# Kernel tuning notes

Hardware: AMD Instinct MI355X
Metric: run time of the kernel (lower is better)

Reference implementation:

```python
import jax, jax.numpy as jnp
import numpy as np
import math

D_K = 128
M_BYTES = 65536  # default M = 1024*64
B_C = math.ceil(M_BYTES / (4 * D_K))  # = 128 key-block size
SCALE = 1.0 / math.sqrt(D_K)


def setup_inputs() -> dict:
    key = jax.random.key(0)
    kq, kk, kv = jax.random.split(key, 3)
    shape = (2, 16, 2048, 128)  # (b, heads, seq, d_k)
    return {
        "Q": jax.random.normal(kq, shape, jnp.float32),
        "K": jax.random.normal(kk, shape, jnp.float32),
        "V": jax.random.normal(kv, shape, jnp.float32),
    }


def reference(Q, K, V):
    b, h, s, d = Q.shape
    nblk = s // B_C
    # [nblk, b, h, B_C, d] key/value blocks, scanned in order (matches outer j loop)
    Kb = jnp.transpose(K.reshape(b, h, nblk, B_C, d), (2, 0, 1, 3, 4))
    Vb = jnp.transpose(V.reshape(b, h, nblk, B_C, d), (2, 0, 1, 3, 4))
    j0s = jnp.arange(nblk) * B_C
    q_pos = jnp.arange(s)[:, None]          # [s,1]
    k_off = jnp.arange(B_C)[None, :]        # [1,B_C]

    O0 = jnp.zeros_like(Q)
    l0 = jnp.zeros((b, h, s, 1), Q.dtype)
    m0 = jnp.full((b, h, s, 1), -jnp.inf, Q.dtype)

    def step(carry, xs):
        O, l, m = carry
        Kj, Vj, j0 = xs
        S_ij = jnp.einsum('bhqd,bhkd->bhqk', Q, Kj) * SCALE  # [b,h,s,B_C]
        mask = (j0 + k_off) > q_pos                           # [s,B_C] causal
        S_ij = jnp.where(mask[None, None], -jnp.inf, S_ij)
        m_ij = S_ij.max(axis=-1, keepdims=True)
        m_new = jnp.maximum(m, m_ij)
        P = jnp.exp(S_ij - m_new)
        e_i = jnp.exp(m - m_new)
        e_ij = jnp.exp(m_ij - m_new)  # NOTE: extra factor, faithful to source's bug
        l_new = e_i * l + P.sum(axis=-1, keepdims=True)
        O_new = (e_i * l * O + e_ij * jnp.einsum('bhqk,bhkd->bhqd', P, Vj)) / l_new
        return (O_new, l_new, m_new), None

    (O, _, _), _ = jax.lax.scan(step, (O0, l0, m0), (Kb, Vb, j0s))
    return O
```

## Files before the change

kernel.cpp:

```cpp
#include <hip/hip_runtime.h>
#include <math.h>


using f16   = _Float16;
using f16x8 = __attribute__((ext_vector_type(8))) _Float16;
using f32x4 = __attribute__((ext_vector_type(4))) float;

#define SEQ 2048
#define DK  128
#define FA_SCALE 0.08838834764831843f

__global__ __launch_bounds__(256) void cvt_k(const float* __restrict__ K,
                                             f16* __restrict__ Kh) {
  int i = blockIdx.x * 256 + threadIdx.x;
  const float4* src = (const float4*)K;
  float4 a = src[2 * i], b = src[2 * i + 1];
  f16x8 h;
  h[0] = (f16)a.x; h[1] = (f16)a.y; h[2] = (f16)a.z; h[3] = (f16)a.w;
  h[4] = (f16)b.x; h[5] = (f16)b.y; h[6] = (f16)b.z; h[7] = (f16)b.w;
  ((f16x8*)Kh)[i] = h;
}

__global__ __launch_bounds__(256) void trans_v(const float* __restrict__ V,
                                               f16* __restrict__ Vtp) {
  __shared__ float Vsh[128][132];
  int st = blockIdx.x, bh = blockIdx.y, tid = threadIdx.x;
  const float* src = V + ((size_t)bh * SEQ + st * 128) * DK;
#pragma unroll
  for (int i = 0; i < 16; ++i) {
    int f = tid + i * 256;
    int k = f >> 5, c = f & 31;
    *(float4*)&Vsh[k][c * 4] = *(const float4*)(src + k * DK + c * 4);
  }
  __syncthreads();
  int d = tid >> 1, hf = tid & 1;
  f16* dst = Vtp + (size_t)bh * DK * SEQ + (size_t)d * SEQ + st * 128 + hf * 64;
#pragma unroll
  for (int i = 0; i < 8; ++i) {
    int s0 = hf * 64 + i * 8;
    int c  = s0 >> 5;
    int lgs = (s0 >> 3) & 3;
    f16x8 hv;
#pragma unroll
    for (int o = 0; o < 8; ++o) {
      int k = (2 * c + (o >> 2)) * 16 + lgs * 4 + (o & 3);
      hv[o] = (f16)Vsh[k][d];
    }
    *(f16x8*)(dst + i * 8) = hv;
  }
}

__device__ __forceinline__ void gl_lds16(const void* g, void* l) {
  __builtin_amdgcn_global_load_lds(
      (const __attribute__((address_space(1))) unsigned int*)g,
      (__attribute__((address_space(3))) unsigned int*)l, 16, 0, 0);
}

__device__ __forceinline__ void stage32k(const char* gbase, size_t gstride,
                                         char* lds, int w, int lg, int ll) {
#pragma unroll
  for (int i = 0; i < 4; ++i) {
    int t = w * 4 + i;
    int row = t * 4 + lg;
    int blog = (ll * 16) ^ ((row & 7) << 4);
    gl_lds16(gbase + (size_t)row * gstride + blog, lds + t * 1024);
  }
}

__global__ __launch_bounds__(512, 2) void fa_fwd_f16(
    const float* __restrict__ Q, const f16* __restrict__ Kh,
    const f16* __restrict__ Vtp, float* __restrict__ O) {
  const int bh = blockIdx.x;
  const int qt = 15 - blockIdx.y;
  const int tid  = threadIdx.x;
  const int lane = tid & 63;
  const int w  = tid >> 6;
  const int ll = lane & 15;
  const int lg = lane >> 4;
  const int swz = (ll & 7) << 4;

  __shared__ __align__(16) f16 Ks[2][128 * 128];
  __shared__ __align__(16) f16 Vs[2][128 * 128];

  const float* QB = Q + (size_t)bh * SEQ * DK;
  const char*  KB = (const char*)(Kh + (size_t)bh * SEQ * DK);
  const char*  VB = (const char*)(Vtp + (size_t)bh * DK * SEQ);
  float*       OB = O + (size_t)bh * SEQ * DK;

  const int qrow = qt * 128 + w * 16 + ll;

  f16x8 qf[4];
#pragma unroll
  for (int dc = 0; dc < 4; ++dc) {
    const float* p = QB + (size_t)qrow * DK + dc * 32 + lg * 8;
    float4 a = *(const float4*)p, b = *(const float4*)(p + 4);
    f16x8 h;
    h[0] = (f16)a.x; h[1] = (f16)a.y; h[2] = (f16)a.z; h[3] = (f16)a.w;
    h[4] = (f16)b.x; h[5] = (f16)b.y; h[6] = (f16)b.z; h[7] = (f16)b.w;
    qf[dc] = h;
  }

  f32x4 u[8];
#pragma unroll
  for (int n = 0; n < 8; ++n) u[n] = 0;
  float m = -INFINITY, lsum = 0.f;

  stage32k(KB, 256, (char*)&Ks[0][0], w, lg, ll);
  stage32k(VB, 4096, (char*)&Vs[0][0], w, lg, ll);
  __syncthreads();

  for (int kb = 0; kb <= qt; ++kb) {
    const int cur = kb & 1;
    if (kb < qt) {
      stage32k(KB + (size_t)(kb + 1) * 32768, 256, (char*)&Ks[cur ^ 1][0], w, lg, ll);
      stage32k(VB + (size_t)(kb + 1) * 256, 4096, (char*)&Vs[cur ^ 1][0], w, lg, ll);
    }

    f32x4 s[8];
#pragma unroll
    for (int k16 = 0; k16 < 8; ++k16) s[k16] = 0;
    const char* Kc = (const char*)&Ks[cur][0];
#pragma unroll
    for (int dc = 0; dc < 4; ++dc) {
      const int boff = (dc * 64 + lg * 16) ^ swz;
#pragma unroll
      for (int k16 = 0; k16 < 8; ++k16) {
        f16x8 kf = *(const f16x8*)(Kc + (k16 * 16 + ll) * 256 + boff);
        s[k16] = __builtin_amdgcn_mfma_f32_16x16x32_f16(kf, qf[dc], s[k16], 0, 0, 0);
      }
    }

    float mx = -INFINITY;
    if (kb == qt) {
      const int kbase = kb * 128;
#pragma unroll
      for (int k16 = 0; k16 < 8; ++k16)
#pragma unroll
        for (int r = 0; r < 4; ++r) {
          float v = s[k16][r] * FA_SCALE;
          if (kbase + k16 * 16 + lg * 4 + r > qrow) v = -INFINITY;
          s[k16][r] = v;
          mx = fmaxf(mx, v);
        }
    } else {
#pragma unroll
      for (int k16 = 0; k16 < 8; ++k16)
#pragma unroll
        for (int r = 0; r < 4; ++r) {
          float v = s[k16][r] * FA_SCALE;
          s[k16][r] = v;
          mx = fmaxf(mx, v);
        }
    }
    mx = fmaxf(mx, __shfl_xor(mx, 16));
    mx = fmaxf(mx, __shfl_xor(mx, 32));

    const float mn = fmaxf(m, mx);
    const float ei = __expf(m - mn);
    const float ej = __expf(mx - mn);
    m = mn;

    float ps = 0.f;
#pragma unroll
    for (int k16 = 0; k16 < 8; ++k16)
#pragma unroll
      for (int r = 0; r < 4; ++r) {
        float p = __expf(s[k16][r] - mn);
        s[k16][r] = p;
        ps += p;
      }
    ps += __shfl_xor(ps, 16);
    ps += __shfl_xor(ps, 32);
    lsum = ei * lsum + ps;

    f16x8 pa[4];
#pragma unroll
    for (int c = 0; c < 4; ++c) {
      f16x8 h;
#pragma unroll
      for (int r = 0; r < 4; ++r) {
        h[r]     = (f16)(s[2 * c][r] * ej);
        h[r + 4] = (f16)(s[2 * c + 1][r] * ej);
      }
      pa[c] = h;
    }

    const float eu0 = __shfl(ei, lg * 4 + 0);
    const float eu1 = __shfl(ei, lg * 4 + 1);
    const float eu2 = __shfl(ei, lg * 4 + 2);
    const float eu3 = __shfl(ei, lg * 4 + 3);
#pragma unroll
    for (int n = 0; n < 8; ++n) {
      u[n][0] *= eu0; u[n][1] *= eu1; u[n][2] *= eu2; u[n][3] *= eu3;
    }

    const char* Vc = (const char*)&Vs[cur][0];
#pragma unroll
    for (int c = 0; c < 4; ++c) {
      const int boff = (c * 64 + lg * 16) ^ swz;
#pragma unroll
      for (int n = 0; n < 8; ++n) {
        f16x8 vf = *(const f16x8*)(Vc + (n * 16 + ll) * 256 + boff);
        u[n] = __builtin_amdgcn_mfma_f32_16x16x32_f16(pa[c], vf, u[n], 0, 0, 0);
      }
    }

    __syncthreads();
  }

  const float rl0 = 1.f / __shfl(lsum, lg * 4 + 0);
  const float rl1 = 1.f / __shfl(lsum, lg * 4 + 1);
  const float rl2 = 1.f / __shfl(lsum, lg * 4 + 2);
  const float rl3 = 1.f / __shfl(lsum, lg * 4 + 3);
  const size_t rbase = (size_t)(qt * 128 + w * 16 + lg * 4);
#pragma unroll
  for (int n = 0; n < 8; ++n) {
    const int col = n * 16 + ll;
    OB[(rbase + 0) * DK + col] = u[n][0] * rl0;
    OB[(rbase + 1) * DK + col] = u[n][1] * rl1;
    OB[(rbase + 2) * DK + col] = u[n][2] * rl2;
    OB[(rbase + 3) * DK + col] = u[n][3] * rl3;
  }
}

extern "C" void kernel_launch(void* const* d_in, const int* in_sizes, int n_in,
                              void* d_out, int out_size, void* d_ws, size_t ws_size,
                              hipStream_t stream) {
  const float* Q = (const float*)d_in[0];
  const float* K = (const float*)d_in[1];
  const float* V = (const float*)d_in[2];
  float* O = (float*)d_out;
  (void)in_sizes; (void)n_in; (void)out_size; (void)ws_size;

  f16* Kh  = (f16*)d_ws;
  f16* Vtp = (f16*)((char*)d_ws + 16777216);

  cvt_k<<<4096, 256, 0, stream>>>(K, Kh);
  trans_v<<<dim3(16, 32), 256, 0, stream>>>(V, Vtp);
  fa_fwd_f16<<<dim3(32, 16), 512, 0, stream>>>(Q, Kh, Vtp, O);
}
```

Before: 194.6 us.

## Fuse K convert and V transpose prep, remap block order, add MFMA priority

```diff
diff --git a/kernel.cpp b/kernel.cpp
--- a/kernel.cpp
+++ b/kernel.cpp
@@ -10,43 +10,49 @@
 #define DK  128
 #define FA_SCALE 0.08838834764831843f
 
-__global__ __launch_bounds__(256) void cvt_k(const float* __restrict__ K,
-                                             f16* __restrict__ Kh) {
-  int i = blockIdx.x * 256 + threadIdx.x;
-  const float4* src = (const float4*)K;
-  float4 a = src[2 * i], b = src[2 * i + 1];
-  f16x8 h;
-  h[0] = (f16)a.x; h[1] = (f16)a.y; h[2] = (f16)a.z; h[3] = (f16)a.w;
-  h[4] = (f16)b.x; h[5] = (f16)b.y; h[6] = (f16)b.z; h[7] = (f16)b.w;
-  ((f16x8*)Kh)[i] = h;
-}
-
-__global__ __launch_bounds__(256) void trans_v(const float* __restrict__ V,
+__global__ __launch_bounds__(256) void prep_kv(const float* __restrict__ K,
+                                               const float* __restrict__ V,
+                                               f16* __restrict__ Kh,
                                                f16* __restrict__ Vtp) {
   __shared__ float Vsh[128][132];
-  int st = blockIdx.x, bh = blockIdx.y, tid = threadIdx.x;
-  const float* src = V + ((size_t)bh * SEQ + st * 128) * DK;
+  const int st = blockIdx.x, bh = blockIdx.y, tid = threadIdx.x;
+  const size_t blk = ((size_t)bh * SEQ + st * 128) * DK;
+
+  const float* Ksrc = K + blk;
+  f16* Kdst = Kh + blk;
+#pragma unroll
+  for (int i = 0; i < 8; ++i) {
+    int u = tid + i * 256;
+    float4 a = *(const float4*)(Ksrc + u * 8);
+    float4 b = *(const float4*)(Ksrc + u * 8 + 4);
+    f16x8 h;
+    h[0] = (f16)a.x; h[1] = (f16)a.y; h[2] = (f16)a.z; h[3] = (f16)a.w;
+    h[4] = (f16)b.x; h[5] = (f16)b.y; h[6] = (f16)b.z; h[7] = (f16)b.w;
+    *(f16x8*)(Kdst + u * 8) = h;
+  }
+
+  const float* Vsrc = V + blk;
 #pragma unroll
   for (int i = 0; i < 16; ++i) {
     int f = tid + i * 256;
     int k = f >> 5, c = f & 31;
-    *(float4*)&Vsh[k][c * 4] = *(const float4*)(src + k * DK + c * 4);
+    *(float4*)&Vsh[k][c * 4] = *(const float4*)(Vsrc + k * DK + c * 4);
   }
   __syncthreads();
-  int d = tid >> 1, hf = tid & 1;
-  f16* dst = Vtp + (size_t)bh * DK * SEQ + (size_t)d * SEQ + st * 128 + hf * 64;
-#pragma unroll
-  for (int i = 0; i < 8; ++i) {
-    int s0 = hf * 64 + i * 8;
-    int c  = s0 >> 5;
-    int lgs = (s0 >> 3) & 3;
-    f16x8 hv;
+
+  const int l = tid & 63, wv = tid >> 6;
+  const int r = l & 15, dr = l >> 4;
+  f16* Vdst = Vtp + (size_t)bh * DK * SEQ + st * 128;
+#pragma unroll
+  for (int it = 0; it < 8; ++it) {
+    int d = wv * 32 + it * 4 + dr;
+    f16x8 h;
 #pragma unroll
     for (int o = 0; o < 8; ++o) {
-      int k = (2 * c + (o >> 2)) * 16 + lgs * 4 + (o & 3);
-      hv[o] = (f16)Vsh[k][d];
-    }
-    *(f16x8*)(dst + i * 8) = hv;
+      int k = 32 * (r >> 2) + 16 * (o >> 2) + 4 * (r & 3) + (o & 3);
+      h[o] = (f16)Vsh[k][d];
+    }
+    *(f16x8*)(Vdst + (size_t)d * SEQ + r * 8) = h;
   }
 }
 
@@ -70,8 +76,11 @@
 __global__ __launch_bounds__(512, 2) void fa_fwd_f16(
     const float* __restrict__ Q, const f16* __restrict__ Kh,
     const f16* __restrict__ Vtp, float* __restrict__ O) {
-  const int bh = blockIdx.x;
-  const int qt = 15 - blockIdx.y;
+  const int n = blockIdx.x;
+  const int m = n >> 3;
+  const int bh = (n & 7) * 4 + (m & 3);
+  const int qt = 15 - (m >> 2);
+
   const int tid  = threadIdx.x;
   const int lane = tid & 63;
   const int w  = tid >> 6;
@@ -102,8 +111,8 @@
 
   f32x4 u[8];
 #pragma unroll
-  for (int n = 0; n < 8; ++n) u[n] = 0;
-  float m = -INFINITY, lsum = 0.f;
+  for (int nn = 0; nn < 8; ++nn) u[nn] = 0;
+  float m_run = -INFINITY, lsum = 0.f;
 
   stage32k(KB, 256, (char*)&Ks[0][0], w, lg, ll);
   stage32k(VB, 4096, (char*)&Vs[0][0], w, lg, ll);
@@ -120,6 +129,7 @@
 #pragma unroll
     for (int k16 = 0; k16 < 8; ++k16) s[k16] = 0;
     const char* Kc = (const char*)&Ks[cur][0];
+    __builtin_amdgcn_s_setprio(1);
 #pragma unroll
     for (int dc = 0; dc < 4; ++dc) {
       const int boff = (dc * 64 + lg * 16) ^ swz;
@@ -129,6 +139,7 @@
         s[k16] = __builtin_amdgcn_mfma_f32_16x16x32_f16(kf, qf[dc], s[k16], 0, 0, 0);
       }
     }
+    __builtin_amdgcn_s_setprio(0);
 
     float mx = -INFINITY;
     if (kb == qt) {
@@ -155,10 +166,10 @@
     mx = fmaxf(mx, __shfl_xor(mx, 16));
     mx = fmaxf(mx, __shfl_xor(mx, 32));
 
-    const float mn = fmaxf(m, mx);
-    const float ei = __expf(m - mn);
+    const float mn = fmaxf(m_run, mx);
+    const float ei = __expf(m_run - mn);
     const float ej = __expf(mx - mn);
-    m = mn;
+    m_run = mn;
 
     float ps = 0.f;
 #pragma unroll
@@ -190,20 +201,22 @@
     const float eu2 = __shfl(ei, lg * 4 + 2);
     const float eu3 = __shfl(ei, lg * 4 + 3);
 #pragma unroll
-    for (int n = 0; n < 8; ++n) {
-      u[n][0] *= eu0; u[n][1] *= eu1; u[n][2] *= eu2; u[n][3] *= eu3;
+    for (int nn = 0; nn < 8; ++nn) {
+      u[nn][0] *= eu0; u[nn][1] *= eu1; u[nn][2] *= eu2; u[nn][3] *= eu3;
     }
 
     const char* Vc = (const char*)&Vs[cur][0];
+    __builtin_amdgcn_s_setprio(1);
 #pragma unroll
     for (int c = 0; c < 4; ++c) {
       const int boff = (c * 64 + lg * 16) ^ swz;
 #pragma unroll
-      for (int n = 0; n < 8; ++n) {
-        f16x8 vf = *(const f16x8*)(Vc + (n * 16 + ll) * 256 + boff);
-        u[n] = __builtin_amdgcn_mfma_f32_16x16x32_f16(pa[c], vf, u[n], 0, 0, 0);
-      }
-    }
+      for (int nn = 0; nn < 8; ++nn) {
+        f16x8 vf = *(const f16x8*)(Vc + (nn * 16 + ll) * 256 + boff);
+        u[nn] = __builtin_amdgcn_mfma_f32_16x16x32_f16(pa[c], vf, u[nn], 0, 0, 0);
+      }
+    }
+    __builtin_amdgcn_s_setprio(0);
 
     __syncthreads();
   }
@@ -214,12 +227,12 @@
   const float rl3 = 1.f / __shfl(lsum, lg * 4 + 3);
   const size_t rbase = (size_t)(qt * 128 + w * 16 + lg * 4);
 #pragma unroll
-  for (int n = 0; n < 8; ++n) {
-    const int col = n * 16 + ll;
-    OB[(rbase + 0) * DK + col] = u[n][0] * rl0;
-    OB[(rbase + 1) * DK + col] = u[n][1] * rl1;
-    OB[(rbase + 2) * DK + col] = u[n][2] * rl2;
-    OB[(rbase + 3) * DK + col] = u[n][3] * rl3;
+  for (int nn = 0; nn < 8; ++nn) {
+    const int col = nn * 16 + ll;
+    OB[(rbase + 0) * DK + col] = u[nn][0] * rl0;
+    OB[(rbase + 1) * DK + col] = u[nn][1] * rl1;
+    OB[(rbase + 2) * DK + col] = u[nn][2] * rl2;
+    OB[(rbase + 3) * DK + col] = u[nn][3] * rl3;
   }
 }
 
@@ -235,7 +248,6 @@
   f16* Kh  = (f16*)d_ws;
   f16* Vtp = (f16*)((char*)d_ws + 16777216);
 
-  cvt_k<<<4096, 256, 0, stream>>>(K, Kh);
-  trans_v<<<dim3(16, 32), 256, 0, stream>>>(V, Vtp);
-  fa_fwd_f16<<<dim3(32, 16), 512, 0, stream>>>(Q, Kh, Vtp, O);
-}
+  prep_kv<<<dim3(16, 32), 256, 0, stream>>>(K, V, Kh, Vtp);
+  fa_fwd_f16<<<512, 512, 0, stream>>>(Q, Kh, Vtp, O);
+}
```

Result: no change. 192.3 us (-1.2%).
